# Kernel optimization log

Measured on AMD Instinct MI355X. Metric: run time of the kernel, lower is better.

The kernel has to match this reference:

```python
import jax, jax.numpy as jnp
import numpy as np

B, C = 4096, 10000


def setup_inputs() -> dict:
    key = jax.random.key(0)
    k1, k2, k3, k4, k5 = jax.random.split(key, 5)
    return {
        "outputs1": jax.random.normal(k1, (B, C), jnp.float32),
        "outputs2": jax.random.normal(k2, (B, C), jnp.float32),
        "outputs3": jax.random.normal(k3, (B, C), jnp.float32),
        "out_s": jax.random.normal(k4, (B, C), jnp.float32),
        "targets": jax.random.randint(k5, (B,), 0, C),
    }


def _margin(out, targets):
    # top1 - top2 if the target class is the argmax, else 0  -> [B]
    top2 = jax.lax.top_k(out, 2)[0]                              # [B, 2]
    tgt = jnp.take_along_axis(out, targets[:, None], axis=1)[:, 0]
    return jnp.where(tgt == top2[:, 0], top2[:, 0] - top2[:, 1], jnp.zeros_like(tgt))


def reference(outputs1, outputs2, outputs3, out_s, targets):
    T_THR = 2.0   # Threshold_weights3 temperature
    T_KD = 20.0   # KL_divergence temperature
    ALPHA = 0.8

    mimic = (outputs1 + outputs2 + outputs3) / 3.0
    teachers = (outputs1, outputs2, outputs3, mimic)

    # per-sample confidence margins for each teacher -> softmax ensemble weights [B,4]
    d = jnp.stack([_margin(t, targets) for t in teachers], axis=1)
    out_threshold = jax.nn.softmax(d / T_THR, axis=1)

    # global max over the three real teachers (scalar)
    max_preds = jnp.maximum(jnp.max(outputs1), jnp.maximum(jnp.max(outputs2), jnp.max(outputs3)))

    # per-sample student CE (shared across teachers)
    ce = -jnp.take_along_axis(jax.nn.log_softmax(out_s, axis=1), targets[:, None], axis=1)[:, 0]
    logp_s = jax.nn.log_softmax(out_s / T_KD, axis=1)

    def loss_for(teacher):
        w = jnp.take_along_axis(teacher, targets[:, None], axis=1)[:, 0] / max_preds
        kd = -jnp.sum(jax.nn.softmax(teacher / T_KD, axis=1) * logp_s, axis=1) * (T_KD * T_KD)
        return (1.0 - ALPHA * w) * ce + (ALPHA * w) * kd

    losses = jnp.stack([loss_for(t) for t in teachers], axis=1)  # [B,4]
    return jnp.mean(jnp.sum(out_threshold * losses, axis=1))
```

## Files before the change

kernel.cpp:

```cpp
#include <hip/hip_runtime.h>

namespace {
constexpr int kB = 4096;
constexpr int kC = 10000;
constexpr int kC4 = kC / 4;
constexpr int kNT = 256;
constexpr int kIters = (kC4 + kNT - 1) / kNT;
}

__device__ __forceinline__ float wave_sum(float v) {
#pragma unroll
  for (int o = 32; o > 0; o >>= 1) v += __shfl_down(v, o, 64);
  return v;
}

__device__ __forceinline__ double wave_sum_d(double v) {
#pragma unroll
  for (int o = 32; o > 0; o >>= 1) v += __shfl_down(v, o, 64);
  return v;
}

__device__ __forceinline__ float wave_max(float v) {
#pragma unroll
  for (int o = 32; o > 0; o >>= 1) v = fmaxf(v, __shfl_down(v, o, 64));
  return v;
}

__device__ __forceinline__ void wave_top2(float& m1, float& m2) {
#pragma unroll
  for (int o = 32; o > 0; o >>= 1) {
    float a1 = __shfl_down(m1, o, 64);
    float a2 = __shfl_down(m2, o, 64);
    float lo = fminf(m1, a1);
    m1 = fmaxf(m1, a1);
    m2 = fmaxf(lo, fmaxf(m2, a2));
  }
}

struct Chunk {
  float4 a, b, c, s;
};

__device__ __forceinline__ void accum_chunk(
    const Chunk& K, float (&m1)[4], float (&m2)[4], float (&Z)[4], float (&D)[4],
    float& Z1, float& Z20) {
  const float va[4] = {K.a.x, K.a.y, K.a.z, K.a.w};
  const float vb[4] = {K.b.x, K.b.y, K.b.z, K.b.w};
  const float vc[4] = {K.c.x, K.c.y, K.c.z, K.c.w};
  const float vs[4] = {K.s.x, K.s.y, K.s.z, K.s.w};
#pragma unroll
  for (int j = 0; j < 4; j++) {
    const float mim = (va[j] + vb[j] + vc[j]) * (1.0f / 3.0f);
    const float tv[4] = {va[j], vb[j], vc[j], mim};
    const float sv = vs[j];
#pragma unroll
    for (int t = 0; t < 4; t++) {
      const float x = tv[t];
      const float lo = fminf(x, m1[t]);
      m1[t] = fmaxf(x, m1[t]);
      m2[t] = fmaxf(m2[t], lo);
      const float e = __expf(x * 0.05f);
      Z[t] += e;
      D[t] = fmaf(e, sv, D[t]);
    }
    Z1 += __expf(sv);
    Z20 += __expf(sv * 0.05f);
  }
}

__global__ __launch_bounds__(kNT) void mt3_row_kernel(
    const float* __restrict__ g1, const float* __restrict__ g2,
    const float* __restrict__ g3, const float* __restrict__ gs,
    const int* __restrict__ gt,
    float* __restrict__ ceArr, float* __restrict__ bArr,
    float* __restrict__ mArr) {
  const int b = blockIdx.x;
  const int tid = threadIdx.x;
  const int lane = tid & 63;
  const int wv = tid >> 6;

  const size_t rowOff = (size_t)b * kC;
  const float4* __restrict__ p1 = reinterpret_cast<const float4*>(g1 + rowOff);
  const float4* __restrict__ p2 = reinterpret_cast<const float4*>(g2 + rowOff);
  const float4* __restrict__ p3 = reinterpret_cast<const float4*>(g3 + rowOff);
  const float4* __restrict__ ps = reinterpret_cast<const float4*>(gs + rowOff);

  const int target = gt[b];

  float tv1 = 0.f, tv2 = 0.f, tv3 = 0.f, tvs = 0.f;
  if (tid == 0) {
    tv1 = g1[rowOff + target];
    tv2 = g2[rowOff + target];
    tv3 = g3[rowOff + target];
    tvs = gs[rowOff + target];
  }

  float m1[4], m2[4], Z[4], D[4];
#pragma unroll
  for (int t = 0; t < 4; t++) { m1[t] = -1e30f; m2[t] = -1e30f; Z[t] = 0.f; D[t] = 0.f; }
  float Z1 = 0.f;
  float Z20 = 0.f;

  Chunk X[3];
  {
    const int i0 = tid;
    const int i1 = tid + kNT;
    X[0].a = p1[i0]; X[0].b = p2[i0]; X[0].c = p3[i0]; X[0].s = ps[i0];
    X[1].a = p1[i1]; X[1].b = p2[i1]; X[1].c = p3[i1]; X[1].s = ps[i1];
  }

#pragma unroll
  for (int k = 0; k < kIters; k++) {
    if (k + 2 < kIters) {
      const int cn = tid + (k + 2) * kNT;
      const int idx = (k + 3 < kIters) ? cn : ((cn < kC4) ? cn : tid);
      Chunk& Xn = X[(k + 2) % 3];
      Xn.a = p1[idx]; Xn.b = p2[idx]; Xn.c = p3[idx]; Xn.s = ps[idx];
    }
    __builtin_amdgcn_sched_barrier(0);

    const int c = tid + k * kNT;
    if (k + 1 < kIters || c < kC4)
      accum_chunk(X[k % 3], m1, m2, Z, D, Z1, Z20);
  }

#pragma unroll
  for (int t = 0; t < 4; t++) {
    Z[t] = wave_sum(Z[t]);
    D[t] = wave_sum(D[t]);
    wave_top2(m1[t], m2[t]);
  }
  Z1 = wave_sum(Z1);
  Z20 = wave_sum(Z20);

  __shared__ float sZ[4][4], sD[4][4], sM1[4][4], sM2[4][4], sZ1[4], sZ20[4];
  if (lane == 0) {
#pragma unroll
    for (int t = 0; t < 4; t++) {
      sZ[t][wv] = Z[t]; sD[t][wv] = D[t];
      sM1[t][wv] = m1[t]; sM2[t][wv] = m2[t];
    }
    sZ1[wv] = Z1; sZ20[wv] = Z20;
  }
  __syncthreads();

  if (tid == 0) {
    float fZ[4], fD[4], fM1[4], fM2[4];
    float fZ1 = 0.f, fZ20 = 0.f;
#pragma unroll
    for (int t = 0; t < 4; t++) { fZ[t] = 0.f; fD[t] = 0.f; fM1[t] = -1e30f; fM2[t] = -1e30f; }
#pragma unroll
    for (int w = 0; w < 4; w++) {
      fZ1 += sZ1[w]; fZ20 += sZ20[w];
#pragma unroll
      for (int t = 0; t < 4; t++) {
        fZ[t] += sZ[t][w];
        fD[t] += sD[t][w];
        const float a1 = sM1[t][w], a2 = sM2[t][w];
        const float lo = fminf(fM1[t], a1);
        fM1[t] = fmaxf(fM1[t], a1);
        fM2[t] = fmaxf(lo, fmaxf(fM2[t], a2));
      }
    }

    const float tvm = (tv1 + tv2 + tv3) * (1.0f / 3.0f);
    const float tval[4] = {tv1, tv2, tv3, tvm};

    const float ce = logf(fZ1) - tvs;
    const float lz20 = logf(fZ20);

    float d[4], kd[4];
#pragma unroll
    for (int t = 0; t < 4; t++) {
      kd[t] = 400.0f * (lz20 - fD[t] / (20.0f * fZ[t]));
      d[t] = (tval[t] == fM1[t]) ? (fM1[t] - fM2[t]) : 0.0f;
    }
    float ew[4], se = 0.f;
#pragma unroll
    for (int t = 0; t < 4; t++) { ew[t] = __expf(d[t] * 0.5f); se += ew[t]; }
    float rowB = 0.f;
#pragma unroll
    for (int t = 0; t < 4; t++) rowB += (ew[t] / se) * tval[t] * (kd[t] - ce);

    ceArr[b] = ce;
    bArr[b] = rowB;
    mArr[b] = fmaxf(fM1[0], fmaxf(fM1[1], fM1[2]));
  }
}

__global__ __launch_bounds__(256) void mt3_finalize(
    const float* __restrict__ ceArr, const float* __restrict__ bArr,
    const float* __restrict__ mArr, float* __restrict__ out) {
  const int tid = threadIdx.x;
  const int lane = tid & 63;
  const int wv = tid >> 6;

  double sc = 0.0, sb = 0.0;
  float mx = -1e30f;
  for (int i = tid; i < kB; i += 256) {
    sc += (double)ceArr[i];
    sb += (double)bArr[i];
    mx = fmaxf(mx, mArr[i]);
  }
  sc = wave_sum_d(sc);
  sb = wave_sum_d(sb);
  mx = wave_max(mx);

  __shared__ double dsc[4], dsb[4];
  __shared__ float dmx[4];
  if (lane == 0) { dsc[wv] = sc; dsb[wv] = sb; dmx[wv] = mx; }
  __syncthreads();
  if (tid == 0) {
    double A = 0.0, Bc = 0.0;
    float M = -1e30f;
#pragma unroll
    for (int w = 0; w < 4; w++) { A += dsc[w]; Bc += dsb[w]; M = fmaxf(M, dmx[w]); }
    out[0] = (float)((A + 0.8 * Bc / (double)M) / (double)kB);
  }
}

extern "C" void kernel_launch(void* const* d_in, const int* in_sizes, int n_in,
                              void* d_out, int out_size, void* d_ws, size_t ws_size,
                              hipStream_t stream) {
  const float* o1 = (const float*)d_in[0];
  const float* o2 = (const float*)d_in[1];
  const float* o3 = (const float*)d_in[2];
  const float* os = (const float*)d_in[3];
  const int* tg = (const int*)d_in[4];

  float* ws = (float*)d_ws;
  float* ceArr = ws;
  float* bArr = ws + kB;
  float* mArr = ws + 2 * kB;

  mt3_row_kernel<<<kB, kNT, 0, stream>>>(o1, o2, o3, os, tg, ceArr, bArr, mArr);
  mt3_finalize<<<1, 256, 0, stream>>>(ceArr, bArr, mArr, (float*)d_out);
}
```

Before: 515.1 us.

## Stage rows through double-buffered LDS with each wave loading one input array

Each of the four waves now streams a single input tensor (teacher 1, 2, 3 or student) into a double-buffered shared-memory tile with four float4 loads per lane. All threads then read the four matching values from LDS to do the fused reduction. The goal is fewer distinct concurrent streams per wave and better memory-level parallelism. In exchange it adds LDS traffic, a __syncthreads per iteration, and loses the three-deep register prefetch.

```diff
diff --git a/kernel.cpp b/kernel.cpp
--- a/kernel.cpp
+++ b/kernel.cpp
@@ -5,7 +5,9 @@
 constexpr int kC = 10000;
 constexpr int kC4 = kC / 4;
 constexpr int kNT = 256;
-constexpr int kIters = (kC4 + kNT - 1) / kNT;
+constexpr int kChunk = 256;
+constexpr int kIters = (kC4 + kChunk - 1) / kChunk;
+constexpr int kTail = kC4 - (kIters - 1) * kChunk;
 }
 
 __device__ __forceinline__ float wave_sum(float v) {
@@ -37,17 +39,14 @@
   }
 }
 
-struct Chunk {
-  float4 a, b, c, s;
-};
-
 __device__ __forceinline__ void accum_chunk(
-    const Chunk& K, float (&m1)[4], float (&m2)[4], float (&Z)[4], float (&D)[4],
+    const float4& Av, const float4& Bv, const float4& Cv, const float4& Sv,
+    float (&m1)[4], float (&m2)[4], float (&Z)[4], float (&D)[4],
     float& Z1, float& Z20) {
-  const float va[4] = {K.a.x, K.a.y, K.a.z, K.a.w};
-  const float vb[4] = {K.b.x, K.b.y, K.b.z, K.b.w};
-  const float vc[4] = {K.c.x, K.c.y, K.c.z, K.c.w};
-  const float vs[4] = {K.s.x, K.s.y, K.s.z, K.s.w};
+  const float va[4] = {Av.x, Av.y, Av.z, Av.w};
+  const float vb[4] = {Bv.x, Bv.y, Bv.z, Bv.w};
+  const float vc[4] = {Cv.x, Cv.y, Cv.z, Cv.w};
+  const float vs[4] = {Sv.x, Sv.y, Sv.z, Sv.w};
 #pragma unroll
   for (int j = 0; j < 4; j++) {
     const float mim = (va[j] + vb[j] + vc[j]) * (1.0f / 3.0f);
@@ -80,10 +79,9 @@
   const int wv = tid >> 6;
 
   const size_t rowOff = (size_t)b * kC;
-  const float4* __restrict__ p1 = reinterpret_cast<const float4*>(g1 + rowOff);
-  const float4* __restrict__ p2 = reinterpret_cast<const float4*>(g2 + rowOff);
-  const float4* __restrict__ p3 = reinterpret_cast<const float4*>(g3 + rowOff);
-  const float4* __restrict__ ps = reinterpret_cast<const float4*>(gs + rowOff);
+  const float* bases[4] = {g1 + rowOff, g2 + rowOff, g3 + rowOff, gs + rowOff};
+  const float4* __restrict__ myArr =
+      reinterpret_cast<const float4*>(bases[wv]);
 
   const int target = gt[b];
 
@@ -101,27 +99,58 @@
   float Z1 = 0.f;
   float Z20 = 0.f;
 
-  Chunk X[3];
+  __shared__ float4 lbuf[2][4][kChunk];
+
   {
-    const int i0 = tid;
-    const int i1 = tid + kNT;
-    X[0].a = p1[i0]; X[0].b = p2[i0]; X[0].c = p3[i0]; X[0].s = ps[i0];
-    X[1].a = p1[i1]; X[1].b = p2[i1]; X[1].c = p3[i1]; X[1].s = ps[i1];
-  }
+    float4 r0 = myArr[lane];
+    float4 r1 = myArr[lane + 64];
+    float4 r2 = myArr[lane + 128];
+    float4 r3 = myArr[lane + 192];
+    lbuf[0][wv][lane      ] = r0;
+    lbuf[0][wv][lane +  64] = r1;
+    lbuf[0][wv][lane + 128] = r2;
+    lbuf[0][wv][lane + 192] = r3;
+  }
+  __syncthreads();
 
 #pragma unroll
   for (int k = 0; k < kIters; k++) {
-    if (k + 2 < kIters) {
-      const int cn = tid + (k + 2) * kNT;
-      const int idx = (k + 3 < kIters) ? cn : ((cn < kC4) ? cn : tid);
-      Chunk& Xn = X[(k + 2) % 3];
-      Xn.a = p1[idx]; Xn.b = p2[idx]; Xn.c = p3[idx]; Xn.s = ps[idx];
-    }
-    __builtin_amdgcn_sched_barrier(0);
-
-    const int c = tid + k * kNT;
-    if (k + 1 < kIters || c < kC4)
-      accum_chunk(X[k % 3], m1, m2, Z, D, Z1, Z20);
+    const int cb = k & 1;
+
+    float4 r0, r1, r2, r3;
+    if (k + 1 < kIters) {
+      const int base = (k + 1) * kChunk + lane;
+      if (k + 1 == kIters - 1) {
+        const int i3 = (base + 192 < kC4) ? (base + 192) : base;
+        r0 = myArr[base];
+        r1 = myArr[base + 64];
+        r2 = myArr[base + 128];
+        r3 = myArr[i3];
+      } else {
+        r0 = myArr[base];
+        r1 = myArr[base + 64];
+        r2 = myArr[base + 128];
+        r3 = myArr[base + 192];
+      }
+      __builtin_amdgcn_sched_barrier(0);
+    }
+
+    if (k != kIters - 1 || tid < kTail) {
+      const float4 Av = lbuf[cb][0][tid];
+      const float4 Bv = lbuf[cb][1][tid];
+      const float4 Cv = lbuf[cb][2][tid];
+      const float4 Sv = lbuf[cb][3][tid];
+      accum_chunk(Av, Bv, Cv, Sv, m1, m2, Z, D, Z1, Z20);
+    }
+
+    if (k + 1 < kIters) {
+      const int nb = (k + 1) & 1;
+      lbuf[nb][wv][lane      ] = r0;
+      lbuf[nb][wv][lane +  64] = r1;
+      lbuf[nb][wv][lane + 128] = r2;
+      lbuf[nb][wv][lane + 192] = r3;
+      __syncthreads();
+    }
   }
 
 #pragma unroll
```

Result: no change. 522.4 us (+1.4%).
